# Performance work log

Measured on AMD Instinct MI355X. Metric: run time of the kernel, lower is better.

The kernel has to match this reference:

```python
import jax, jax.numpy as jnp
import numpy as np


def setup_inputs() -> dict:
    key = jax.random.key(0)
    k1, k2, k3, k4 = jax.random.split(key, 4)
    B, M, S, Q = 128, 200, 20, 20
    H, V, D = 3, 50000, 128  # max_hops, num_vocab, embedding_dim
    story = jax.random.randint(k1, (B, M, S), 0, V)
    query = jax.random.randint(k2, (B, Q), 0, V)
    # (max_hops+1) embedding tables, init normal(0, 0.1) as in torch code
    E = jax.random.normal(k3, (H + 1, V, D), dtype=jnp.float32) * 0.1
    # (max_hops+1) temporal encodings [max_story_size, D], normal(0, 0.1)
    T = jax.random.normal(k4, (H + 1, M, D), dtype=jnp.float32) * 0.1
    return {"story": story, "query": query, "E": E, "T": T}


def reference(story, query, E, T):
    max_hops = E.shape[0] - 1
    # u1 = sum over query tokens of B-embedding (hop-0 table)
    u = jnp.sum(E[0][query], axis=1)  # [B, D]
    for hop in range(max_hops):
        # memory: A-embed story, sum over words, add temporal encoding
        m = jnp.sum(E[hop][story], axis=2) + T[hop]        # [B, M, D]
        # attention over memories (legacy F.softmax on 2D -> dim=1)
        uTm = jnp.einsum('bmd,bd->bm', m, u)               # [B, M]
        proba = jax.nn.softmax(uTm, axis=1)
        # output memory representation
        c = jnp.sum(E[hop + 1][story], axis=2) + T[hop + 1]  # [B, M, D]
        o = jnp.einsum('bm,bmd->bd', proba, c)             # [B, D]
        u = u + o
    ahat = u @ E[-1].T  # [B, V]
    return ahat, jax.nn.softmax(ahat, axis=1)
```

## Files before the change

### kernel.cpp

```cpp
#include <hip/hip_runtime.h>
#include <float.h>


constexpr int Bn = 128;
constexpr int Mn = 200;
constexpr int Sn = 20;
constexpr int Qn = 20;
constexpr int Hn = 3;
constexpr int Vn = 50000;
constexpr int Dn = 128;
constexpr int CH = 100;

constexpr size_t MSUM_ELEMS = (size_t)(Hn + 1) * Bn * Mn * Dn;

typedef float  f32x4 __attribute__((ext_vector_type(4)));
typedef int    i32x4 __attribute__((ext_vector_type(4)));

__global__ __launch_bounds__(256)
void msum_table_kernel(const int* __restrict__ story, const float4* __restrict__ Et,
                       const float4* __restrict__ Tt, float4* __restrict__ msumT) {
    int slot = threadIdx.x >> 5;
    int l    = threadIdx.x & 31;
    int rbm  = blockIdx.x * 8 + slot;
    int m    = rbm % Mn;

    const i32x4* st4 = (const i32x4*)(story + (size_t)rbm * Sn);
    i32x4 iv0 = __builtin_nontemporal_load(st4 + 0);
    i32x4 iv1 = __builtin_nontemporal_load(st4 + 1);
    i32x4 iv2 = __builtin_nontemporal_load(st4 + 2);
    i32x4 iv3 = __builtin_nontemporal_load(st4 + 3);
    i32x4 iv4 = __builtin_nontemporal_load(st4 + 4);
    int idx[Sn] = {iv0.x, iv0.y, iv0.z, iv0.w, iv1.x, iv1.y, iv1.z, iv1.w,
                   iv2.x, iv2.y, iv2.z, iv2.w, iv3.x, iv3.y, iv3.z, iv3.w,
                   iv4.x, iv4.y, iv4.z, iv4.w};

    f32x4 acc = __builtin_nontemporal_load((const f32x4*)Tt + (size_t)m * 32 + l);
    #pragma unroll
    for (int s = 0; s < Sn; ++s) {
        float4 e = Et[(size_t)idx[s] * 32 + l];
        acc.x += e.x; acc.y += e.y; acc.z += e.z; acc.w += e.w;
    }
    __builtin_nontemporal_store(acc, (f32x4*)msumT + (size_t)rbm * 32 + l);
}

__global__ __launch_bounds__(1024)
void hops_kernel(const int* __restrict__ query, const float* __restrict__ E,
                 const float* __restrict__ msum, float* __restrict__ ufin) {
    __shared__ float u[Dn];
    __shared__ float sc[Mn];
    __shared__ float op[8 * Dn];
    __shared__ float red[16];
    __shared__ float bc[2];

    const int b    = blockIdx.x;
    const int tid  = threadIdx.x;
    const int wave = tid >> 6;
    const int lane = tid & 63;
    const int d    = tid & (Dn - 1);
    const int g    = tid >> 7;

    if (tid < Dn) {
        float acc = 0.f;
        const int* q = query + b * Qn;
        #pragma unroll
        for (int j = 0; j < Qn; ++j)
            acc += E[(size_t)q[j] * Dn + tid];
        u[tid] = acc;
    }
    __syncthreads();

    for (int hop = 0; hop < Hn; ++hop) {
        const float* mrow = msum + ((size_t)hop * Bn + b) * (size_t)(Mn * Dn);
        float ul = u[lane], uh = u[lane + 64];

        for (int mm = wave; mm < Mn / 2; mm += 16) {
            const float* r0 = mrow + (2 * mm) * Dn;
            const float* r1 = r0 + Dn;
            float p0 = r0[lane] * ul + r0[lane + 64] * uh;
            float p1 = r1[lane] * ul + r1[lane + 64] * uh;
            #pragma unroll
            for (int off = 32; off; off >>= 1) {
                p0 += __shfl_down(p0, off, 64);
                p1 += __shfl_down(p1, off, 64);
            }
            if (lane == 0) { sc[2 * mm] = p0; sc[2 * mm + 1] = p1; }
        }
        __syncthreads();

        float v = (tid < Mn) ? sc[tid] : -FLT_MAX;
        float mx = v;
        #pragma unroll
        for (int off = 32; off; off >>= 1) mx = fmaxf(mx, __shfl_down(mx, off, 64));
        if (lane == 0) red[wave] = mx;
        __syncthreads();
        if (tid == 0) {
            float m0 = red[0];
            #pragma unroll
            for (int i = 1; i < 16; ++i) m0 = fmaxf(m0, red[i]);
            bc[0] = m0;
        }
        __syncthreads();
        float rmax = bc[0];
        float e = (tid < Mn) ? expf(v - rmax) : 0.f;
        float sm = e;
        #pragma unroll
        for (int off = 32; off; off >>= 1) sm += __shfl_down(sm, off, 64);
        if (lane == 0) red[wave] = sm;
        __syncthreads();
        if (tid == 0) {
            float s = 0.f;
            #pragma unroll
            for (int i = 0; i < 16; ++i) s += red[i];
            bc[1] = s;
        }
        __syncthreads();
        float inv = 1.f / bc[1];
        if (tid < Mn) sc[tid] = e * inv;
        __syncthreads();

        const float* crow = msum + ((size_t)(hop + 1) * Bn + b) * (size_t)(Mn * Dn);
        float acc = 0.f;
        for (int m = g; m < Mn; m += 8)
            acc += sc[m] * crow[m * Dn + d];
        op[g * Dn + d] = acc;
        __syncthreads();
        if (tid < Dn) {
            float s = 0.f;
            #pragma unroll
            for (int i = 0; i < 8; ++i) s += op[i * Dn + tid];
            u[tid] += s;
        }
        __syncthreads();
    }
    if (tid < Dn) ufin[b * Dn + tid] = u[tid];
}

__global__ __launch_bounds__(1024)
void hops_fused_kernel(const int* __restrict__ story, const int* __restrict__ query,
                       const float* __restrict__ E, const float* __restrict__ T,
                       float* __restrict__ ufin) {
    __shared__ __align__(16) float tile[CH * Dn];
    __shared__ float u[Dn];
    __shared__ float sc[Mn];
    __shared__ float op[8 * Dn];
    __shared__ float red[16];
    __shared__ float bc[2];

    const int b    = blockIdx.x;
    const int tid  = threadIdx.x;
    const int wave = tid >> 6;
    const int lane = tid & 63;
    const int d    = tid & (Dn - 1);
    const int g    = tid >> 7;
    const int slot = tid >> 5;
    const int l    = tid & 31;
    const int* st  = story + b * (Mn * Sn);

    if (tid < Dn) {
        float acc = 0.f;
        const int* q = query + b * Qn;
        #pragma unroll
        for (int j = 0; j < Qn; ++j)
            acc += E[(size_t)q[j] * Dn + tid];
        u[tid] = acc;
    }

    auto build = [&](int t, int base) {
        const float4* Et = (const float4*)(E) + (size_t)t * Vn * 32;
        const float4* Tt = (const float4*)(T) + (size_t)t * Mn * 32;
        for (int m = base + slot; m < base + CH; m += 32) {
            const int* sm = st + m * Sn;
            float4 acc = Tt[(size_t)m * 32 + l];
            #pragma unroll
            for (int s = 0; s < Sn; ++s) {
                float4 e = Et[(size_t)sm[s] * 32 + l];
                acc.x += e.x; acc.y += e.y; acc.z += e.z; acc.w += e.w;
            }
            ((float4*)tile)[(m - base) * 32 + l] = acc;
        }
    };
    auto scores = [&](int base) {
        for (int m = base + wave; m < base + CH; m += 16) {
            float p = tile[(m - base) * Dn + lane]      * u[lane]
                    + tile[(m - base) * Dn + lane + 64] * u[lane + 64];
            #pragma unroll
            for (int off = 32; off; off >>= 1) p += __shfl_down(p, off, 64);
            if (lane == 0) sc[m] = p;
        }
    };

    for (int hop = 0; hop < Hn; ++hop) {
        if (hop == 0) {
            build(0, 0);  __syncthreads(); scores(0);  __syncthreads();
            build(0, CH); __syncthreads(); scores(CH); __syncthreads();
        } else {
            scores(CH); __syncthreads();
            build(hop, 0); __syncthreads(); scores(0); __syncthreads();
        }

        float v = (tid < Mn) ? sc[tid] : -FLT_MAX;
        float mx = v;
        #pragma unroll
        for (int off = 32; off; off >>= 1) mx = fmaxf(mx, __shfl_down(mx, off, 64));
        if (lane == 0) red[wave] = mx;
        __syncthreads();
        if (tid == 0) {
            float m0 = red[0];
            #pragma unroll
            for (int i = 1; i < 16; ++i) m0 = fmaxf(m0, red[i]);
            bc[0] = m0;
        }
        __syncthreads();
        float rmax = bc[0];
        float e = (tid < Mn) ? expf(v - rmax) : 0.f;
        float sm = e;
        #pragma unroll
        for (int off = 32; off; off >>= 1) sm += __shfl_down(sm, off, 64);
        if (lane == 0) red[wave] = sm;
        __syncthreads();
        if (tid == 0) {
            float s = 0.f;
            #pragma unroll
            for (int i = 0; i < 16; ++i) s += red[i];
            bc[1] = s;
        }
        __syncthreads();
        float inv = 1.f / bc[1];
        if (tid < Mn) sc[tid] = e * inv;

        float oacc = 0.f;
        build(hop + 1, 0);
        __syncthreads();
        for (int m = g; m < CH; m += 8)
            oacc += sc[m] * tile[m * Dn + d];
        __syncthreads();
        build(hop + 1, CH);
        __syncthreads();
        for (int m = CH + g; m < 2 * CH; m += 8)
            oacc += sc[m] * tile[(m - CH) * Dn + d];
        op[g * Dn + d] = oacc;
        __syncthreads();
        if (tid < Dn) {
            float s = 0.f;
            #pragma unroll
            for (int i = 0; i < 8; ++i) s += op[i * Dn + tid];
            u[tid] += s;
        }
        __syncthreads();
    }

    if (tid < Dn) ufin[b * Dn + tid] = u[tid];
}

constexpr int KC   = 32;
constexpr int LSTR = 140;
__device__ __forceinline__ int ldsCol(int c) { return c + 4 * (c >> 5); }

__global__ __launch_bounds__(256)
void ahat_gemm_kernel(const float* __restrict__ E, const float* __restrict__ ufin,
                      float* __restrict__ out) {
    __shared__ float uA[KC * LSTR];
    __shared__ float eB[KC * LSTR];
    const float* E3 = E + (size_t)Hn * Vn * Dn;

    const int tid   = threadIdx.x;
    const int tr    = tid & 15;
    const int tc    = tid >> 4;
    const int vbase = blockIdx.x * 128;

    const int f4 = tid & 7;
    const int rr = tid >> 3;

    float acc[8][8];
    #pragma unroll
    for (int i = 0; i < 8; ++i)
        #pragma unroll
        for (int j = 0; j < 8; ++j) acc[i][j] = 0.f;

    for (int kb = 0; kb < Dn; kb += KC) {
        #pragma unroll
        for (int i = 0; i < 4; ++i) {
            int r   = rr + 32 * i;
            int col = ldsCol(r);
            float4 uv = *(const float4*)(ufin + (size_t)r * Dn + kb + f4 * 4);
            uA[(f4 * 4 + 0) * LSTR + col] = uv.x;
            uA[(f4 * 4 + 1) * LSTR + col] = uv.y;
            uA[(f4 * 4 + 2) * LSTR + col] = uv.z;
            uA[(f4 * 4 + 3) * LSTR + col] = uv.w;
            int vg = vbase + r; if (vg > Vn - 1) vg = Vn - 1;
            float4 ev = *(const float4*)(E3 + (size_t)vg * Dn + kb + f4 * 4);
            eB[(f4 * 4 + 0) * LSTR + col] = ev.x;
            eB[(f4 * 4 + 1) * LSTR + col] = ev.y;
            eB[(f4 * 4 + 2) * LSTR + col] = ev.z;
            eB[(f4 * 4 + 3) * LSTR + col] = ev.w;
        }
        __syncthreads();
        const int ca = ldsCol(tr * 8);
        const int cb = ldsCol(tc * 8);
        #pragma unroll 2
        for (int k = 0; k < KC; ++k) {
            float4 a0 = *(const float4*)&uA[k * LSTR + ca];
            float4 a1 = *(const float4*)&uA[k * LSTR + ca + 4];
            float4 b0 = *(const float4*)&eB[k * LSTR + cb];
            float4 b1 = *(const float4*)&eB[k * LSTR + cb + 4];
            float av[8] = {a0.x, a0.y, a0.z, a0.w, a1.x, a1.y, a1.z, a1.w};
            float bv[8] = {b0.x, b0.y, b0.z, b0.w, b1.x, b1.y, b1.z, b1.w};
            #pragma unroll
            for (int i = 0; i < 8; ++i)
                #pragma unroll
                for (int j = 0; j < 8; ++j)
                    acc[i][j] += av[i] * bv[j];
        }
        __syncthreads();
    }

    const int v0 = vbase + tc * 8;
    if (v0 < Vn) {
        #pragma unroll
        for (int i = 0; i < 8; ++i) {
            int bb = tr * 8 + i;
            *(float4*)(out + (size_t)bb * Vn + v0) =
                make_float4(acc[i][0], acc[i][1], acc[i][2], acc[i][3]);
            *(float4*)(out + (size_t)bb * Vn + v0 + 4) =
                make_float4(acc[i][4], acc[i][5], acc[i][6], acc[i][7]);
        }
    }
}

__global__ __launch_bounds__(1024)
void softmax_kernel(const float* __restrict__ ahat, float* __restrict__ osm) {
    __shared__ float redm[16];
    __shared__ float reds[16];
    __shared__ float bc2[2];

    int b    = blockIdx.x;
    int tid  = threadIdx.x;
    int wave = tid >> 6;
    int lane = tid & 63;

    const float4* row  = (const float4*)(ahat + (size_t)b * Vn);
    float4*       orow = (float4*)(osm + (size_t)b * Vn);
    constexpr int N4 = Vn / 4;

    float m = -FLT_MAX, s = 0.f;
    for (int v = tid; v < N4; v += 1024) {
        float4 x = row[v];
        float cm = fmaxf(fmaxf(x.x, x.y), fmaxf(x.z, x.w));
        if (cm > m) { s *= __expf(m - cm); m = cm; }
        s += __expf(x.x - m) + __expf(x.y - m) + __expf(x.z - m) + __expf(x.w - m);
    }
    #pragma unroll
    for (int off = 32; off; off >>= 1) {
        float mo = __shfl_down(m, off, 64);
        float so = __shfl_down(s, off, 64);
        float nm = fmaxf(m, mo);
        s = s * __expf(m - nm) + so * __expf(mo - nm);
        m = nm;
    }
    if (lane == 0) { redm[wave] = m; reds[wave] = s; }
    __syncthreads();
    if (tid == 0) {
        float M = redm[0];
        #pragma unroll
        for (int i = 1; i < 16; ++i) M = fmaxf(M, redm[i]);
        float S = 0.f;
        #pragma unroll
        for (int i = 0; i < 16; ++i) S += reds[i] * __expf(redm[i] - M);
        bc2[0] = M; bc2[1] = 1.f / S;
    }
    __syncthreads();
    float rmax = bc2[0];
    float inv  = bc2[1];

    for (int v = tid; v < N4; v += 1024) {
        float4 x = row[v];
        orow[v] = make_float4(__expf(x.x - rmax) * inv, __expf(x.y - rmax) * inv,
                              __expf(x.z - rmax) * inv, __expf(x.w - rmax) * inv);
    }
}

extern "C" void kernel_launch(void* const* d_in, const int* in_sizes, int n_in,
                              void* d_out, int out_size, void* d_ws, size_t ws_size,
                              hipStream_t stream) {
    const int*   story = (const int*)d_in[0];
    const int*   query = (const int*)d_in[1];
    const float* E     = (const float*)d_in[2];
    const float* T     = (const float*)d_in[3];

    float* out  = (float*)d_out;
    float* ufin = out + (size_t)Bn * Vn;

    if (ws_size >= MSUM_ELEMS * sizeof(float)) {
        float* msum = (float*)d_ws;
        for (int t = 0; t < Hn + 1; ++t) {
            msum_table_kernel<<<Bn * Mn / 8, 256, 0, stream>>>(
                story,
                (const float4*)(E + (size_t)t * Vn * Dn),
                (const float4*)(T + (size_t)t * Mn * Dn),
                (float4*)(msum + (size_t)t * Bn * Mn * Dn));
        }
        hops_kernel<<<Bn, 1024, 0, stream>>>(query, E, msum, ufin);
    } else {
        hops_fused_kernel<<<Bn, 1024, 0, stream>>>(story, query, E, T, ufin);
    }
    ahat_gemm_kernel<<<(Vn + 127) / 128, 256, 0, stream>>>(E, ufin, out);
    softmax_kernel<<<Bn, 1024, 0, stream>>>(out, out + (size_t)Bn * Vn);
}
```

Measured before the change: 382.9 us.

## Fuse per-tile softmax statistics into GEMM epilogue and merge softmax in one pass

The GEMM epilogue now computes each tile's per-row max and sum-exp and writes them to workspace. A new merge kernel combines those partials and normalizes each row chunk in a grid of chunks by batch, which drops one full read pass over the logits. Alongside this, the four per-table msum launches become a single launch, the hop score loop uses float2 loads over four rows at a time, and the attention softmax switches to the fast __expf. The new path costs extra workspace and needs enough ws_size to be taken, otherwise it falls back to the old softmax.

```diff
diff --git a/kernel.cpp b/kernel.cpp
--- a/kernel.cpp
+++ b/kernel.cpp
@@ -11,42 +11,41 @@
 constexpr int Dn = 128;
 constexpr int CH = 100;
 
+constexpr int GTILE = 128;
+constexpr int NT    = (Vn + GTILE - 1) / GTILE;
+constexpr int SMCHK = 10;
+
 constexpr size_t MSUM_ELEMS = (size_t)(Hn + 1) * Bn * Mn * Dn;
-
-typedef float  f32x4 __attribute__((ext_vector_type(4)));
-typedef int    i32x4 __attribute__((ext_vector_type(4)));
+constexpr size_t SMWS_ELEMS = (size_t)NT * Bn * 2;
 
 __global__ __launch_bounds__(256)
-void msum_table_kernel(const int* __restrict__ story, const float4* __restrict__ Et,
-                       const float4* __restrict__ Tt, float4* __restrict__ msumT) {
+void msum_kernel(const int* __restrict__ story, const float* __restrict__ E,
+                 const float* __restrict__ T, float* __restrict__ msum) {
     int slot = threadIdx.x >> 5;
     int l    = threadIdx.x & 31;
-    int rbm  = blockIdx.x * 8 + slot;
-    int m    = rbm % Mn;
-
-    const i32x4* st4 = (const i32x4*)(story + (size_t)rbm * Sn);
-    i32x4 iv0 = __builtin_nontemporal_load(st4 + 0);
-    i32x4 iv1 = __builtin_nontemporal_load(st4 + 1);
-    i32x4 iv2 = __builtin_nontemporal_load(st4 + 2);
-    i32x4 iv3 = __builtin_nontemporal_load(st4 + 3);
-    i32x4 iv4 = __builtin_nontemporal_load(st4 + 4);
-    int idx[Sn] = {iv0.x, iv0.y, iv0.z, iv0.w, iv1.x, iv1.y, iv1.z, iv1.w,
-                   iv2.x, iv2.y, iv2.z, iv2.w, iv3.x, iv3.y, iv3.z, iv3.w,
-                   iv4.x, iv4.y, iv4.z, iv4.w};
-
-    f32x4 acc = __builtin_nontemporal_load((const f32x4*)Tt + (size_t)m * 32 + l);
+    int row  = blockIdx.x * 8 + slot;
+    int t    = row / (Bn * Mn);
+    int rem  = row - t * (Bn * Mn);
+    int b    = rem / Mn;
+    int m    = rem - b * Mn;
+
+    const int* st = story + (b * Mn + m) * Sn;
+    const float4* Tv = (const float4*)(T) + (size_t)(t * Mn + m) * 32;
+    const float4* Et = (const float4*)(E) + (size_t)t * Vn * 32;
+
+    float4 acc = Tv[l];
     #pragma unroll
     for (int s = 0; s < Sn; ++s) {
-        float4 e = Et[(size_t)idx[s] * 32 + l];
+        float4 e = Et[(size_t)st[s] * 32 + l];
         acc.x += e.x; acc.y += e.y; acc.z += e.z; acc.w += e.w;
     }
-    __builtin_nontemporal_store(acc, (f32x4*)msumT + (size_t)rbm * 32 + l);
+    ((float4*)msum)[(size_t)row * 32 + l] = acc;
 }
 
 __global__ __launch_bounds__(1024)
 void hops_kernel(const int* __restrict__ query, const float* __restrict__ E,
                  const float* __restrict__ msum, float* __restrict__ ufin) {
-    __shared__ float u[Dn];
+    __shared__ __align__(16) float u[Dn];
     __shared__ float sc[Mn];
     __shared__ float op[8 * Dn];
     __shared__ float red[16];
@@ -71,19 +70,29 @@
 
     for (int hop = 0; hop < Hn; ++hop) {
         const float* mrow = msum + ((size_t)hop * Bn + b) * (size_t)(Mn * Dn);
-        float ul = u[lane], uh = u[lane + 64];
-
-        for (int mm = wave; mm < Mn / 2; mm += 16) {
-            const float* r0 = mrow + (2 * mm) * Dn;
-            const float* r1 = r0 + Dn;
-            float p0 = r0[lane] * ul + r0[lane + 64] * uh;
-            float p1 = r1[lane] * ul + r1[lane + 64] * uh;
+        float2 u2 = *(const float2*)(u + 2 * lane);
+
+        for (int q = wave; q < Mn / 4; q += 16) {
+            const float* r = mrow + (size_t)q * 4 * Dn;
+            float2 a0 = *(const float2*)(r + 0 * Dn + 2 * lane);
+            float2 a1 = *(const float2*)(r + 1 * Dn + 2 * lane);
+            float2 a2 = *(const float2*)(r + 2 * Dn + 2 * lane);
+            float2 a3 = *(const float2*)(r + 3 * Dn + 2 * lane);
+            float p0 = a0.x * u2.x + a0.y * u2.y;
+            float p1 = a1.x * u2.x + a1.y * u2.y;
+            float p2 = a2.x * u2.x + a2.y * u2.y;
+            float p3 = a3.x * u2.x + a3.y * u2.y;
             #pragma unroll
             for (int off = 32; off; off >>= 1) {
                 p0 += __shfl_down(p0, off, 64);
                 p1 += __shfl_down(p1, off, 64);
+                p2 += __shfl_down(p2, off, 64);
+                p3 += __shfl_down(p3, off, 64);
             }
-            if (lane == 0) { sc[2 * mm] = p0; sc[2 * mm + 1] = p1; }
+            if (lane == 0) {
+                sc[4 * q + 0] = p0; sc[4 * q + 1] = p1;
+                sc[4 * q + 2] = p2; sc[4 * q + 3] = p3;
+            }
         }
         __syncthreads();
 
@@ -101,7 +110,7 @@
         }
         __syncthreads();
         float rmax = bc[0];
-        float e = (tid < Mn) ? expf(v - rmax) : 0.f;
+        float e = (tid < Mn) ? __expf(v - rmax) : 0.f;
         float sm = e;
         #pragma unroll
         for (int off = 32; off; off >>= 1) sm += __shfl_down(sm, off, 64);
@@ -212,7 +221,7 @@
         }
         __syncthreads();
         float rmax = bc[0];
-        float e = (tid < Mn) ? expf(v - rmax) : 0.f;
+        float e = (tid < Mn) ? __expf(v - rmax) : 0.f;
         float sm = e;
         #pragma unroll
         for (int off = 32; off; off >>= 1) sm += __shfl_down(sm, off, 64);
@@ -258,15 +267,15 @@
 
 __global__ __launch_bounds__(256)
 void ahat_gemm_kernel(const float* __restrict__ E, const float* __restrict__ ufin,
-                      float* __restrict__ out) {
-    __shared__ float uA[KC * LSTR];
-    __shared__ float eB[KC * LSTR];
+                      float* __restrict__ out, float* __restrict__ ws2) {
+    __shared__ __align__(16) float uA[KC * LSTR];
+    __shared__ __align__(16) float eB[KC * LSTR];
     const float* E3 = E + (size_t)Hn * Vn * Dn;
 
     const int tid   = threadIdx.x;
     const int tr    = tid & 15;
     const int tc    = tid >> 4;
-    const int vbase = blockIdx.x * 128;
+    const int vbase = blockIdx.x * GTILE;
 
     const int f4 = tid & 7;
     const int rr = tid >> 3;
@@ -287,7 +296,12 @@
             uA[(f4 * 4 + 1) * LSTR + col] = uv.y;
             uA[(f4 * 4 + 2) * LSTR + col] = uv.z;
             uA[(f4 * 4 + 3) * LSTR + col] = uv.w;
+        }
+        #pragma unroll
+        for (int i = 0; i < 4; ++i) {
+            int r  = rr + 32 * i;
             int vg = vbase + r; if (vg > Vn - 1) vg = Vn - 1;
+            int col = ldsCol(r);
             float4 ev = *(const float4*)(E3 + (size_t)vg * Dn + kb + f4 * 4);
             eB[(f4 * 4 + 0) * LSTR + col] = ev.x;
             eB[(f4 * 4 + 1) * LSTR + col] = ev.y;
@@ -314,8 +328,9 @@
         __syncthreads();
     }
 
-    const int v0 = vbase + tc * 8;
-    if (v0 < Vn) {
+    const int  v0    = vbase + tc * 8;
+    const bool valid = v0 < Vn;
+    if (valid) {
         #pragma unroll
         for (int i = 0; i < 8; ++i) {
             int bb = tr * 8 + i;
@@ -325,29 +340,54 @@
                 make_float4(acc[i][4], acc[i][5], acc[i][6], acc[i][7]);
         }
     }
-}
-
-__global__ __launch_bounds__(1024)
-void softmax_kernel(const float* __restrict__ ahat, float* __restrict__ osm) {
-    __shared__ float redm[16];
-    __shared__ float reds[16];
-    __shared__ float bc2[2];
-
-    int b    = blockIdx.x;
-    int tid  = threadIdx.x;
-    int wave = tid >> 6;
-    int lane = tid & 63;
-
-    const float4* row  = (const float4*)(ahat + (size_t)b * Vn);
-    float4*       orow = (float4*)(osm + (size_t)b * Vn);
-    constexpr int N4 = Vn / 4;
+
+    if (ws2) {
+        #pragma unroll
+        for (int i = 0; i < 8; ++i) {
+            float tm = -FLT_MAX, ts = 0.f;
+            if (valid) {
+                #pragma unroll
+                for (int j = 0; j < 8; ++j) tm = fmaxf(tm, acc[i][j]);
+                #pragma unroll
+                for (int j = 0; j < 8; ++j) ts += __expf(acc[i][j] - tm);
+            }
+            uA[tc * 128 + tr * 8 + i] = tm;
+            eB[tc * 128 + tr * 8 + i] = ts;
+        }
+        __syncthreads();
+        if (tid < Bn) {
+            float M = -FLT_MAX;
+            #pragma unroll
+            for (int t = 0; t < 16; ++t) M = fmaxf(M, uA[t * 128 + tid]);
+            float S = 0.f;
+            #pragma unroll
+            for (int t = 0; t < 16; ++t)
+                S += eB[t * 128 + tid] * __expf(uA[t * 128 + tid] - M);
+            float2* w = (float2*)ws2;
+            w[(size_t)blockIdx.x * Bn + tid] = make_float2(M, S);
+        }
+    }
+}
+
+__global__ __launch_bounds__(256)
+void softmax_merge_kernel(const float* __restrict__ ahat, const float* __restrict__ ws2,
+                          float* __restrict__ osm) {
+    __shared__ float redm[4], reds[4];
+    __shared__ float bcM, bcI;
+
+    const int ck   = blockIdx.x;
+    const int b    = blockIdx.y;
+    const int tid  = threadIdx.x;
+    const int wave = tid >> 6;
+    const int lane = tid & 63;
 
     float m = -FLT_MAX, s = 0.f;
-    for (int v = tid; v < N4; v += 1024) {
-        float4 x = row[v];
-        float cm = fmaxf(fmaxf(x.x, x.y), fmaxf(x.z, x.w));
-        if (cm > m) { s *= __expf(m - cm); m = cm; }
-        s += __expf(x.x - m) + __expf(x.y - m) + __expf(x.z - m) + __expf(x.w - m);
+    const float2* w = (const float2*)ws2;
+    for (int i = tid; i < NT; i += 256) {
+        float2 p = w[(size_t)i * Bn + b];
+        float nm = fmaxf(m, p.x);
+        s = s * __expf(m - nm) + p.y * __expf(p.x - nm);
+        m = nm;
     }
     #pragma unroll
     for (int off = 32; off; off >>= 1) {
@@ -362,6 +402,61 @@
     if (tid == 0) {
         float M = redm[0];
         #pragma unroll
+        for (int i = 1; i < 4; ++i) M = fmaxf(M, redm[i]);
+        float S = 0.f;
+        #pragma unroll
+        for (int i = 0; i < 4; ++i) S += reds[i] * __expf(redm[i] - M);
+        bcM = M; bcI = 1.f / S;
+    }
+    __syncthreads();
+    const float M   = bcM;
+    const float inv = bcI;
+
+    constexpr int C4 = Vn / SMCHK / 4;
+    const float4* row  = (const float4*)(ahat + (size_t)b * Vn) + (size_t)ck * C4;
+    float4*       orow = (float4*)(osm + (size_t)b * Vn) + (size_t)ck * C4;
+    for (int v = tid; v < C4; v += 256) {
+        float4 x = row[v];
+        orow[v] = make_float4(__expf(x.x - M) * inv, __expf(x.y - M) * inv,
+                              __expf(x.z - M) * inv, __expf(x.w - M) * inv);
+    }
+}
+
+__global__ __launch_bounds__(1024)
+void softmax_kernel(const float* __restrict__ ahat, float* __restrict__ osm) {
+    __shared__ float redm[16];
+    __shared__ float reds[16];
+    __shared__ float bc2[2];
+
+    int b    = blockIdx.x;
+    int tid  = threadIdx.x;
+    int wave = tid >> 6;
+    int lane = tid & 63;
+
+    const float4* row  = (const float4*)(ahat + (size_t)b * Vn);
+    float4*       orow = (float4*)(osm + (size_t)b * Vn);
+    constexpr int N4 = Vn / 4;
+
+    float m = -FLT_MAX, s = 0.f;
+    for (int v = tid; v < N4; v += 1024) {
+        float4 x = row[v];
+        float cm = fmaxf(fmaxf(x.x, x.y), fmaxf(x.z, x.w));
+        if (cm > m) { s *= __expf(m - cm); m = cm; }
+        s += __expf(x.x - m) + __expf(x.y - m) + __expf(x.z - m) + __expf(x.w - m);
+    }
+    #pragma unroll
+    for (int off = 32; off; off >>= 1) {
+        float mo = __shfl_down(m, off, 64);
+        float so = __shfl_down(s, off, 64);
+        float nm = fmaxf(m, mo);
+        s = s * __expf(m - nm) + so * __expf(mo - nm);
+        m = nm;
+    }
+    if (lane == 0) { redm[wave] = m; reds[wave] = s; }
+    __syncthreads();
+    if (tid == 0) {
+        float M = redm[0];
+        #pragma unroll
         for (int i = 1; i < 16; ++i) M = fmaxf(M, redm[i]);
         float S = 0.f;
         #pragma unroll
@@ -390,19 +485,24 @@
     float* out  = (float*)d_out;
     float* ufin = out + (size_t)Bn * Vn;
 
-    if (ws_size >= MSUM_ELEMS * sizeof(float)) {
-        float* msum = (float*)d_ws;
-        for (int t = 0; t < Hn + 1; ++t) {
-            msum_table_kernel<<<Bn * Mn / 8, 256, 0, stream>>>(
-                story,
-                (const float4*)(E + (size_t)t * Vn * Dn),
-                (const float4*)(T + (size_t)t * Mn * Dn),
-                (float4*)(msum + (size_t)t * Bn * Mn * Dn));
-        }
+    const bool haveMsum = ws_size >= MSUM_ELEMS * sizeof(float);
+    const bool haveSm   = ws_size >= (MSUM_ELEMS + SMWS_ELEMS) * sizeof(float);
+    float* msum = (float*)d_ws;
+    float* ws2  = haveSm ? ((float*)d_ws + MSUM_ELEMS) : nullptr;
+
+    if (haveMsum) {
+        msum_kernel<<<(Hn + 1) * Bn * Mn / 8, 256, 0, stream>>>(story, E, T, msum);
         hops_kernel<<<Bn, 1024, 0, stream>>>(query, E, msum, ufin);
     } else {
         hops_fused_kernel<<<Bn, 1024, 0, stream>>>(story, query, E, T, ufin);
     }
-    ahat_gemm_kernel<<<(Vn + 127) / 128, 256, 0, stream>>>(E, ufin, out);
-    softmax_kernel<<<Bn, 1024, 0, stream>>>(out, out + (size_t)Bn * Vn);
-}
+
+    ahat_gemm_kernel<<<NT, 256, 0, stream>>>(E, ufin, out, ws2);
+
+    if (ws2) {
+        softmax_merge_kernel<<<dim3(SMCHK, Bn), 256, 0, stream>>>(
+            out, ws2, out + (size_t)Bn * Vn);
+    } else {
+        softmax_kernel<<<Bn, 1024, 0, stream>>>(out, out + (size_t)Bn * Vn);
+    }
+}
```

Result: faster. 341.3 us (-10.9%).
